# Kernel tuning notes

Measured on AMD Instinct MI355X. Metric: run time of the kernel, lower is better.

Reference implementation:

```python
import jax, jax.numpy as jnp
import numpy as np

DIM = 1024
SEQ = 8192
BATCH = 4
HID = 128
TARGET_RATIO = 0.5
MIN_SEQ_LEN = 2048


def setup_inputs() -> dict:
    key = jax.random.key(0)
    k0, k1, k2, k3, k4 = jax.random.split(key, 5)
    x = jax.random.normal(k0, (BATCH, SEQ, DIM), dtype=jnp.float32)
    # torch.nn.Linear default init: U(-1/sqrt(fan_in), 1/sqrt(fan_in))
    s1 = 1.0 / np.sqrt(DIM)
    s2 = 1.0 / np.sqrt(HID)
    W1 = jax.random.uniform(k1, (DIM, HID), jnp.float32, -s1, s1)
    b1 = jax.random.uniform(k2, (HID,), jnp.float32, -s1, s1)
    W2 = jax.random.uniform(k3, (HID, 1), jnp.float32, -s2, s2)
    b2 = jax.random.uniform(k4, (1,), jnp.float32, -s2, s2)
    return {"x": x, "W1": W1, "b1": b1, "W2": W2, "b2": b2}


def reference(x, W1, b1, W2, b2):
    B, S, D = x.shape
    # importance scorer: Linear -> GELU (exact, matching torch nn.GELU) -> Linear, squeeze(-1)
    h = jax.nn.gelu(jnp.einsum('bsd,dh->bsh', x, W1) + b1, approximate=False)
    scores = (jnp.einsum('bsh,ho->bso', h, W2) + b2)[..., 0]  # [B, S]

    # keep_ratio = max(0.1, target_ratio * min(1, min_seq_len / seq_len))
    length_factor = min(1.0, MIN_SEQ_LEN / S)
    keep_ratio = max(0.1, TARGET_RATIO * length_factor)
    num_keep = max(1, int(S * keep_ratio))  # static at trace time

    _, indices = jax.lax.top_k(scores, num_keep)       # [B, num_keep]
    indices = jnp.sort(indices, axis=1)                # restore temporal order
    kept_tokens = jnp.take_along_axis(x, indices[..., None], axis=1)  # [B, num_keep, D]
    return kept_tokens, indices
```

## Files before the change

### kernel.cpp

```cpp
#include <hip/hip_runtime.h>
#include <hip/hip_bf16.h>

#define DIMD 1024
#define HIDD 128
#define SEQ  8192
#define BATCH 4
#define KEEP 1024

typedef __attribute__((ext_vector_type(8))) short short8;
typedef __attribute__((ext_vector_type(8))) _Float16 f16x8;
typedef __attribute__((ext_vector_type(4))) float f32x4;
typedef __attribute__((ext_vector_type(4))) unsigned int u32x4;

__device__ __forceinline__ float gelu_exact(float h) {
    return 0.5f * h * (1.0f + erff(h * 0.70710678118654752440f));
}
__device__ __forceinline__ void gload_lds16(const void* g, void* l) {
    __builtin_amdgcn_global_load_lds(
        (const __attribute__((address_space(1))) void*)g,
        (__attribute__((address_space(3))) void*)l, 16, 0, 0);
}

__global__ __launch_bounds__(256)
void w1split_kernel(const float* __restrict__ W1, char* __restrict__ img) {
    const int t = blockIdx.x * 256 + threadIdx.x;
    const int c = t & 127;
    const int j = (t >> 7) & 7;
    const int kt = t >> 10;
    f16x8 hv, lv;
#pragma unroll
    for (int i = 0; i < 8; ++i) {
        const float f = W1[(kt * 64 + j * 8 + i) * 128 + c];
        const _Float16 h = (_Float16)f;
        const _Float16 l = (_Float16)((f - (float)h) * 4096.0f);
        hv[i] = h; lv[i] = l;
    }
    const int off = kt * 16384 + c * 128 + 16 * (j ^ (c & 7));
    *(f16x8*)(img + off) = hv;
    *(f16x8*)(img + 262144 + off) = lv;
}

__global__ __launch_bounds__(256, 3)
void score_mfma(const float* __restrict__ x, const char* __restrict__ w1img,
                const float* __restrict__ b1, const float* __restrict__ W2,
                const float* __restrict__ b2, float* __restrict__ scores) {
    __shared__ __align__(16) char lds[49152];
    char* const Ah = lds;
    char* const Al = lds + 8192;
    char* const Bh = lds + 16384;
    char* const Bl = lds + 32768;

    const int tid = threadIdx.x;
    const int lane = tid & 63;
    const int wid = tid >> 6;
    const int wm = wid >> 1;
    const int wn = wid & 1;
    const long rowBase = (long)blockIdx.x * 64;

    f32x4 acc[2][4], acc2[2][4];
#pragma unroll
    for (int m = 0; m < 2; ++m)
#pragma unroll
        for (int n = 0; n < 4; ++n) {
            acc[m][n] = (f32x4){0.f, 0.f, 0.f, 0.f};
            acc2[m][n] = (f32x4){0.f, 0.f, 0.f, 0.f};
        }

    for (int kt = 0; kt < DIMD; kt += 64) {
        __syncthreads();
        {
            const long tbase = (long)(kt >> 6) * 16384;
#pragma unroll
            for (int i = 0; i < 4; ++i) {
                const int off = wid * 4096 + i * 1024;
                gload_lds16(w1img + tbase + off + lane * 16, Bh + off);
                gload_lds16(w1img + 262144 + tbase + off + lane * 16, Bl + off);
            }
        }
        {
            const int row = tid >> 2, q = tid & 3;
            const float* gx = x + (rowBase + row) * DIMD + kt + q * 16;
#pragma unroll
            for (int j = 0; j < 2; ++j) {
                const f32x4 v0 = *(const f32x4*)(gx + j * 8);
                const f32x4 v1 = *(const f32x4*)(gx + j * 8 + 4);
                f16x8 hv, lv;
#pragma unroll
                for (int i = 0; i < 4; ++i) {
                    const _Float16 h0 = (_Float16)v0[i];
                    const _Float16 h1 = (_Float16)v1[i];
                    hv[i] = h0; hv[4 + i] = h1;
                    lv[i] = (_Float16)((v0[i] - (float)h0) * 4096.0f);
                    lv[4 + i] = (_Float16)((v1[i] - (float)h1) * 4096.0f);
                }
                const int kb = q * 32 + j * 16;
                const int off = row * 128 + (kb ^ ((row & 7) << 4));
                *(f16x8*)(Ah + off) = hv;
                *(f16x8*)(Al + off) = lv;
            }
        }
        __syncthreads();

#pragma unroll
        for (int ks = 0; ks < 2; ++ks) {
            const int kbase = ks * 64 + (lane >> 4) * 16;
            f16x8 ah[2], al[2];
#pragma unroll
            for (int m = 0; m < 2; ++m) {
                const int row = wm * 32 + m * 16 + (lane & 15);
                const int off = row * 128 + (kbase ^ ((row & 7) << 4));
                ah[m] = *(const f16x8*)(Ah + off);
                al[m] = *(const f16x8*)(Al + off);
            }
#pragma unroll
            for (int n = 0; n < 4; ++n) {
                const int col = wn * 64 + n * 16 + (lane & 15);
                const int off = col * 128 + (kbase ^ ((col & 7) << 4));
                const f16x8 bh = *(const f16x8*)(Bh + off);
                const f16x8 bl = *(const f16x8*)(Bl + off);
#pragma unroll
                for (int m = 0; m < 2; ++m) {
                    acc[m][n]  = __builtin_amdgcn_mfma_f32_16x16x32_f16(ah[m], bh, acc[m][n], 0, 0, 0);
                    acc2[m][n] = __builtin_amdgcn_mfma_f32_16x16x32_f16(ah[m], bl, acc2[m][n], 0, 0, 0);
                    acc2[m][n] = __builtin_amdgcn_mfma_f32_16x16x32_f16(al[m], bh, acc2[m][n], 0, 0, 0);
                }
            }
        }
    }

    float rsum[2][4];
#pragma unroll
    for (int m = 0; m < 2; ++m)
#pragma unroll
        for (int r = 0; r < 4; ++r) rsum[m][r] = 0.f;
#pragma unroll
    for (int n = 0; n < 4; ++n) {
        const int col = wn * 64 + n * 16 + (lane & 15);
        const float b1c = b1[col], w2c = W2[col];
#pragma unroll
        for (int m = 0; m < 2; ++m)
#pragma unroll
            for (int r = 0; r < 4; ++r) {
                const float h = acc[m][n][r] + 2.44140625e-4f * acc2[m][n][r] + b1c;
                rsum[m][r] += gelu_exact(h) * w2c;
            }
    }
#pragma unroll
    for (int m = 0; m < 2; ++m)
#pragma unroll
        for (int r = 0; r < 4; ++r) {
#pragma unroll
            for (int o = 1; o < 16; o <<= 1)
                rsum[m][r] += __shfl_xor(rsum[m][r], o, 64);
        }
    __syncthreads();
    float* scpad = (float*)lds;
    if ((lane & 15) == 0) {
#pragma unroll
        for (int m = 0; m < 2; ++m)
#pragma unroll
            for (int r = 0; r < 4; ++r) {
                const int row = wm * 32 + m * 16 + (lane >> 4) * 4 + r;
                scpad[wn * 64 + row] = rsum[m][r];
            }
    }
    __syncthreads();
    if (tid < 64)
        scores[rowBase + tid] = scpad[tid] + scpad[64 + tid] + b2[0];
}

__device__ __forceinline__ unsigned sortable_u32(float f) {
    unsigned u = __float_as_uint(f);
    return (u & 0x80000000u) ? ~u : (u | 0x80000000u);
}

__global__ __launch_bounds__(1024)
void select_kernel(const float* __restrict__ scores, int* __restrict__ idx_out,
                   float* __restrict__ out_tail) {
    const int b = blockIdx.x;
    const int t = threadIdx.x;
    const int wave = t >> 6, lane = t & 63;

    __shared__ unsigned wh[16 * 256];
    __shared__ unsigned wsum[16];
    __shared__ unsigned sbc_bin, sbc_sub;

    unsigned key[8];
    {
        const float* sc = scores + b * SEQ + t * 8;
        f32x4 v0 = *(const f32x4*)(sc);
        f32x4 v1 = *(const f32x4*)(sc + 4);
#pragma unroll
        for (int i = 0; i < 4; ++i) {
            key[i] = sortable_u32(v0[i]);
            key[4 + i] = sortable_u32(v1[i]);
        }
    }

    unsigned prefix = 0, need = KEEP;
    for (int r = 0; r < 4; ++r) {
        const int shift = 24 - 8 * r;
        const unsigned mask_hi = (r == 0) ? 0u : (0xFFFFFFFFu << (shift + 8));
#pragma unroll
        for (int i = 0; i < 4; ++i) wh[t + i * 1024] = 0;
        __syncthreads();
#pragma unroll
        for (int j = 0; j < 8; ++j)
            if ((key[j] & mask_hi) == prefix)
                atomicAdd(&wh[wave * 256 + ((key[j] >> shift) & 255u)], 1u);
        __syncthreads();
        if (t < 256) {
            unsigned s = 0;
#pragma unroll
            for (int w = 0; w < 16; ++w) s += wh[w * 256 + t];
            wh[t] = s;
        }
        __syncthreads();
        if (wave == 0) {
            const unsigned h0 = wh[lane * 4 + 0], h1 = wh[lane * 4 + 1];
            const unsigned h2 = wh[lane * 4 + 2], h3 = wh[lane * 4 + 3];
            const unsigned s3 = h3, s2 = h2 + s3, s1 = h1 + s2, s0 = h0 + s1;
            unsigned run = s0;
#pragma unroll
            for (int d = 1; d < 64; d <<= 1) {
                const unsigned v = __shfl_down(run, d, 64);
                if (lane + d < 64) run += v;
            }
            const unsigned above = run - s0;
            const unsigned suf0 = above + s0, suf1 = above + s1;
            const unsigned suf2 = above + s2, suf3 = above + s3;
            if (suf1 < need && need <= suf0) { sbc_bin = lane * 4 + 0; sbc_sub = suf1; }
            if (suf2 < need && need <= suf1) { sbc_bin = lane * 4 + 1; sbc_sub = suf2; }
            if (suf3 < need && need <= suf2) { sbc_bin = lane * 4 + 2; sbc_sub = suf3; }
            if (above < need && need <= suf3) { sbc_bin = lane * 4 + 3; sbc_sub = above; }
        }
        __syncthreads();
        prefix |= sbc_bin << shift;
        need -= sbc_sub;
        __syncthreads();
    }
    const unsigned tau = prefix;
    const unsigned m = need;

    unsigned pk[8], tsum = 0;
#pragma unroll
    for (int j = 0; j < 8; ++j) {
        const unsigned gt = (key[j] > tau) ? 1u : 0u;
        const unsigned eq = (key[j] == tau) ? 1u : 0u;
        pk[j] = tsum;
        tsum += (gt << 16) | eq;
    }
    unsigned incl = tsum;
#pragma unroll
    for (int d = 1; d < 64; d <<= 1) {
        const unsigned v = __shfl_up(incl, d, 64);
        if (lane >= d) incl += v;
    }
    if (lane == 63) wsum[wave] = incl;
    __syncthreads();
    if (t == 0) {
        unsigned run = 0;
        for (int w = 0; w < 16; ++w) { const unsigned tmp = wsum[w]; wsum[w] = run; run += tmp; }
    }
    __syncthreads();
    const unsigned base = wsum[wave] + (incl - tsum);

#pragma unroll
    for (int j = 0; j < 8; ++j) {
        const unsigned before = base + pk[j];
        const unsigned gt_before = before >> 16;
        const unsigned eq_before = before & 0xFFFFu;
        const bool keep = (key[j] > tau) || (key[j] == tau && eq_before < m);
        if (keep) {
            const unsigned pos = gt_before + (eq_before < m ? eq_before : m);
            const int idx = t * 8 + j;
            idx_out[b * KEEP + pos] = idx;
            out_tail[b * KEEP + pos] = (float)idx;
        }
    }
}

__global__ __launch_bounds__(256)
void gather_kernel(const float* __restrict__ x, const int* __restrict__ idx,
                   float* __restrict__ out) {
    const int j = blockIdx.x;
    const int b = j >> 10;
    const int id = idx[j];
    const f32x4* src = (const f32x4*)(x + ((long)b * SEQ + id) * DIMD);
    f32x4* dst = (f32x4*)(out + (long)j * DIMD);
    dst[threadIdx.x] = src[threadIdx.x];
}

extern "C" void kernel_launch(void* const* d_in, const int* in_sizes, int n_in,
                              void* d_out, int out_size, void* d_ws, size_t ws_size,
                              hipStream_t stream) {
    const float* x  = (const float*)d_in[0];
    const float* W1 = (const float*)d_in[1];
    const float* b1 = (const float*)d_in[2];
    const float* W2 = (const float*)d_in[3];
    const float* b2 = (const float*)d_in[4];
    float* out = (float*)d_out;

    char* ws = (char*)d_ws;
    char*  w1img  = ws;
    float* scores = (float*)(ws + 524288);
    int*   idxbuf = (int*)(ws + 524288 + 131072);

    w1split_kernel<<<64, 256, 0, stream>>>(W1, w1img);
    score_mfma<<<(BATCH * SEQ) / 64, 256, 0, stream>>>(x, w1img, b1, W2, b2, scores);
    select_kernel<<<BATCH, 1024, 0, stream>>>(scores, idxbuf,
                                              out + (long)BATCH * KEEP * DIMD);
    gather_kernel<<<BATCH * KEEP, 256, 0, stream>>>(x, idxbuf, out);
}
```

Baseline: 229.7 us.

## Double-buffer W1 tiles in LDS and prefetch x tiles into registers

The scoring GEMM loop now stages W1 hi/lo tiles into two alternating LDS buffers and issues the next tile's loads before computing on the current one. The x tile for the next step is prefetched into registers and converted to the split fp16 hi/lo form before each compute phase. This is meant to hide global load latency behind the MFMA work. LDS use grows from 48 KB to 80 KB and launch bounds drop from 3 to 2 blocks per CU, so there is less occupancy to hide latency in other ways. The last step also loads a wrapped-around tile it never uses.

```diff
diff --git a/kernel.cpp b/kernel.cpp
--- a/kernel.cpp
+++ b/kernel.cpp
@@ -40,15 +40,17 @@
     *(f16x8*)(img + 262144 + off) = lv;
 }
 
-__global__ __launch_bounds__(256, 3)
+__global__ __launch_bounds__(256, 2)
 void score_mfma(const float* __restrict__ x, const char* __restrict__ w1img,
                 const float* __restrict__ b1, const float* __restrict__ W2,
                 const float* __restrict__ b2, float* __restrict__ scores) {
-    __shared__ __align__(16) char lds[49152];
-    char* const Ah = lds;
-    char* const Al = lds + 8192;
-    char* const Bh = lds + 16384;
-    char* const Bl = lds + 32768;
+    __shared__ __align__(16) char lds[81920];
+    char* const Ah  = lds;
+    char* const Al  = lds + 8192;
+    char* const Bh0 = lds + 16384;
+    char* const Bl0 = lds + 32768;
+    char* const Bh1 = lds + 49152;
+    char* const Bl1 = lds + 65536;
 
     const int tid = threadIdx.x;
     const int lane = tid & 63;
@@ -57,6 +59,9 @@
     const int wn = wid & 1;
     const long rowBase = (long)blockIdx.x * 64;
 
+    const int arow = tid >> 2, aq = tid & 3;
+    const float* gxBase = x + (rowBase + arow) * DIMD + aq * 16;
+
     f32x4 acc[2][4], acc2[2][4];
 #pragma unroll
     for (int m = 0; m < 2; ++m)
@@ -66,67 +71,91 @@
             acc2[m][n] = (f32x4){0.f, 0.f, 0.f, 0.f};
         }
 
-    for (int kt = 0; kt < DIMD; kt += 64) {
-        __syncthreads();
-        {
-            const long tbase = (long)(kt >> 6) * 16384;
-#pragma unroll
-            for (int i = 0; i < 4; ++i) {
-                const int off = wid * 4096 + i * 1024;
-                gload_lds16(w1img + tbase + off + lane * 16, Bh + off);
-                gload_lds16(w1img + 262144 + tbase + off + lane * 16, Bl + off);
-            }
-        }
-        {
-            const int row = tid >> 2, q = tid & 3;
-            const float* gx = x + (rowBase + row) * DIMD + kt + q * 16;
-#pragma unroll
-            for (int j = 0; j < 2; ++j) {
-                const f32x4 v0 = *(const f32x4*)(gx + j * 8);
-                const f32x4 v1 = *(const f32x4*)(gx + j * 8 + 4);
-                f16x8 hv, lv;
-#pragma unroll
-                for (int i = 0; i < 4; ++i) {
-                    const _Float16 h0 = (_Float16)v0[i];
-                    const _Float16 h1 = (_Float16)v1[i];
-                    hv[i] = h0; hv[4 + i] = h1;
-                    lv[i] = (_Float16)((v0[i] - (float)h0) * 4096.0f);
-                    lv[4 + i] = (_Float16)((v1[i] - (float)h1) * 4096.0f);
-                }
-                const int kb = q * 32 + j * 16;
-                const int off = row * 128 + (kb ^ ((row & 7) << 4));
-                *(f16x8*)(Ah + off) = hv;
-                *(f16x8*)(Al + off) = lv;
-            }
-        }
-        __syncthreads();
-
-#pragma unroll
-        for (int ks = 0; ks < 2; ++ks) {
-            const int kbase = ks * 64 + (lane >> 4) * 16;
-            f16x8 ah[2], al[2];
-#pragma unroll
-            for (int m = 0; m < 2; ++m) {
-                const int row = wm * 32 + m * 16 + (lane & 15);
-                const int off = row * 128 + (kbase ^ ((row & 7) << 4));
-                ah[m] = *(const f16x8*)(Ah + off);
-                al[m] = *(const f16x8*)(Al + off);
-            }
-#pragma unroll
-            for (int n = 0; n < 4; ++n) {
-                const int col = wn * 64 + n * 16 + (lane & 15);
-                const int off = col * 128 + (kbase ^ ((col & 7) << 4));
-                const f16x8 bh = *(const f16x8*)(Bh + off);
-                const f16x8 bl = *(const f16x8*)(Bl + off);
-#pragma unroll
-                for (int m = 0; m < 2; ++m) {
-                    acc[m][n]  = __builtin_amdgcn_mfma_f32_16x16x32_f16(ah[m], bh, acc[m][n], 0, 0, 0);
-                    acc2[m][n] = __builtin_amdgcn_mfma_f32_16x16x32_f16(ah[m], bl, acc2[m][n], 0, 0, 0);
-                    acc2[m][n] = __builtin_amdgcn_mfma_f32_16x16x32_f16(al[m], bh, acc2[m][n], 0, 0, 0);
-                }
-            }
-        }
-    }
+#define STAGE_B(dstH, dstL, tb_) do {                                          \
+    const long _tb = (long)(tb_) * 16384;                                      \
+    _Pragma("unroll")                                                          \
+    for (int i_ = 0; i_ < 4; ++i_) {                                           \
+        const int off_ = wid * 4096 + i_ * 1024;                               \
+        gload_lds16(w1img + _tb + off_ + lane * 16, (dstH) + off_);            \
+        gload_lds16(w1img + 262144 + _tb + off_ + lane * 16, (dstL) + off_);   \
+    } } while (0)
+
+#define LOAD_A(kt_) do {                                                       \
+    const float* _g = gxBase + (kt_);                                          \
+    _Pragma("unroll")                                                          \
+    for (int i_ = 0; i_ < 4; ++i_) ra[i_] = *(const f32x4*)(_g + i_ * 4);      \
+    } while (0)
+
+#define CONV_WRITE() do {                                                      \
+    _Pragma("unroll")                                                          \
+    for (int j_ = 0; j_ < 2; ++j_) {                                           \
+        f16x8 hv_, lv_;                                                        \
+        _Pragma("unroll")                                                      \
+        for (int i_ = 0; i_ < 4; ++i_) {                                       \
+            const float a0_ = ra[2 * j_][i_], a1_ = ra[2 * j_ + 1][i_];        \
+            const _Float16 h0_ = (_Float16)a0_, h1_ = (_Float16)a1_;           \
+            hv_[i_] = h0_; hv_[4 + i_] = h1_;                                  \
+            lv_[i_] = (_Float16)((a0_ - (float)h0_) * 4096.0f);                \
+            lv_[4 + i_] = (_Float16)((a1_ - (float)h1_) * 4096.0f);            \
+        }                                                                      \
+        const int off_ = arow * 128 + ((aq * 32 + j_ * 16) ^ ((arow & 7) << 4));\
+        *(f16x8*)(Ah + off_) = hv_;                                            \
+        *(f16x8*)(Al + off_) = lv_;                                            \
+    } } while (0)
+
+#define COMPUTE(BhC, BlC) do {                                                 \
+    _Pragma("unroll")                                                          \
+    for (int ks_ = 0; ks_ < 2; ++ks_) {                                        \
+        const int kbase_ = ks_ * 64 + (lane >> 4) * 16;                        \
+        f16x8 ahf_[2], alf_[2];                                                \
+        _Pragma("unroll")                                                      \
+        for (int m_ = 0; m_ < 2; ++m_) {                                       \
+            const int r_ = wm * 32 + m_ * 16 + (lane & 15);                    \
+            const int off_ = r_ * 128 + (kbase_ ^ ((r_ & 7) << 4));            \
+            ahf_[m_] = *(const f16x8*)(Ah + off_);                             \
+            alf_[m_] = *(const f16x8*)(Al + off_);                             \
+        }                                                                      \
+        _Pragma("unroll")                                                      \
+        for (int n_ = 0; n_ < 4; ++n_) {                                       \
+            const int c_ = wn * 64 + n_ * 16 + (lane & 15);                    \
+            const int off_ = c_ * 128 + (kbase_ ^ ((c_ & 7) << 4));            \
+            const f16x8 bhf_ = *(const f16x8*)((BhC) + off_);                  \
+            const f16x8 blf_ = *(const f16x8*)((BlC) + off_);                  \
+            _Pragma("unroll")                                                  \
+            for (int m_ = 0; m_ < 2; ++m_) {                                   \
+                acc[m_][n_]  = __builtin_amdgcn_mfma_f32_16x16x32_f16(ahf_[m_], bhf_, acc[m_][n_], 0, 0, 0); \
+                acc2[m_][n_] = __builtin_amdgcn_mfma_f32_16x16x32_f16(ahf_[m_], blf_, acc2[m_][n_], 0, 0, 0); \
+                acc2[m_][n_] = __builtin_amdgcn_mfma_f32_16x16x32_f16(alf_[m_], bhf_, acc2[m_][n_], 0, 0, 0); \
+            }                                                                  \
+        }                                                                      \
+    } } while (0)
+
+#define ITER(t_, BhC, BlC, BhN, BlN) do {                                      \
+    STAGE_B(BhN, BlN, ((t_) + 1) & 15);            \
+    CONV_WRITE();                     \
+    LOAD_A((((t_) + 1) & 15) * 64);                 \
+    asm volatile("s_waitcnt lgkmcnt(0)" ::: "memory");                         \
+    __builtin_amdgcn_s_barrier();                                              \
+    __builtin_amdgcn_sched_barrier(0);                                         \
+    COMPUTE(BhC, BlC);                                                         \
+    asm volatile("s_waitcnt lgkmcnt(0)" ::: "memory");                         \
+    __builtin_amdgcn_s_barrier();                                              \
+    __builtin_amdgcn_sched_barrier(0);                                         \
+    } while (0)
+
+    f32x4 ra[4];
+    STAGE_B(Bh0, Bl0, 0);
+    LOAD_A(0);
+
+    for (int t2 = 0; t2 < 16; t2 += 2) {
+        ITER(t2,     Bh0, Bl0, Bh1, Bl1);
+        ITER(t2 + 1, Bh1, Bl1, Bh0, Bl0);
+    }
+#undef ITER
+#undef COMPUTE
+#undef CONV_WRITE
+#undef LOAD_A
+#undef STAGE_B
 
     float rsum[2][4];
 #pragma unroll
```

Result: no change. 232.8 us (+1.3%).
